# Kernel optimization log

Hardware: AMD Instinct MI355X
Metric: run time of the kernel (lower is better)

The kernel has to match this reference:

```python
import math
import jax, jax.numpy as jnp
import numpy as np

N_EMBD = 768
N_HEAD = 12
BLOCK_SIZE = 1024
B, T, N_ENC = 8, 1024, 257
EPS = 1e-5


def _ln(x, g, b):
    m = jnp.mean(x, axis=-1, keepdims=True)
    v = jnp.var(x, axis=-1, keepdims=True)
    return (x - m) * jax.lax.rsqrt(v + EPS) * g + b


def _heads(t, n_head):
    B_, N_, C_ = t.shape
    return t.reshape(B_, N_, n_head, C_ // n_head).transpose(0, 2, 1, 3)  # [B,H,N,D]


def setup_inputs() -> dict:
    key = jax.random.key(0)
    ks = jax.random.split(key, 16)
    s = 0.02
    d, h4, dq = N_EMBD, 4 * N_EMBD, N_EMBD // 4
    inp = {
        'x': jax.random.normal(ks[0], (B, T, d), jnp.float32),
        'x_enc': jax.random.normal(ks[1], (B, N_ENC, d), jnp.float32),
        'ln1_g': jnp.ones((d,), jnp.float32), 'ln1_b': jnp.zeros((d,), jnp.float32),
        'ln2_g': jnp.ones((d,), jnp.float32), 'ln2_b': jnp.zeros((d,), jnp.float32),
        'ln3_g': jnp.ones((d,), jnp.float32), 'ln3_b': jnp.zeros((d,), jnp.float32),
        'attn_w': jax.random.normal(ks[2], (d, 3 * d), jnp.float32) * s,
        'attn_bias': jnp.zeros((3 * d,), jnp.float32),
        'attn_proj_w': jax.random.normal(ks[3], (d, d), jnp.float32) * s,
        'attn_proj_b': jnp.zeros((d,), jnp.float32),
        'img_w': jax.random.normal(ks[4], (d, 2 * d), jnp.float32) * s,
        'img_b': jnp.zeros((2 * d,), jnp.float32),
        'cap_w': jax.random.normal(ks[5], (d, d), jnp.float32) * s,
        'cap_b': jnp.zeros((d,), jnp.float32),
        'cross_proj_w': jax.random.normal(ks[6], (d, d), jnp.float32) * s,
        'cross_proj_b': jnp.zeros((d,), jnp.float32),
        'ad1_w': jax.random.normal(ks[7], (d, dq), jnp.float32) * s,
        'ad1_b': jnp.zeros((dq,), jnp.float32),
        'ad2_w': jax.random.normal(ks[8], (dq, d), jnp.float32) * s,
        'ad2_b': jnp.zeros((d,), jnp.float32),
        'fc_w': jax.random.normal(ks[9], (d, h4), jnp.float32) * s,
        'fc_b': jnp.zeros((h4,), jnp.float32),
        'mproj_w': jax.random.normal(ks[10], (h4, d), jnp.float32) * s,
        'mproj_b': jnp.zeros((d,), jnp.float32),
    }
    return inp


def _block(x, x_enc, ln1_g, ln1_b, ln2_g, ln2_b, ln3_g, ln3_b,
           attn_w, attn_bias, attn_proj_w, attn_proj_b,
           img_w, img_b, cap_w, cap_b, cross_proj_w, cross_proj_b,
           ad1_w, ad1_b, ad2_w, ad2_b, fc_w, fc_b, mproj_w, mproj_b):
    d, nh = N_EMBD, N_HEAD
    hd = d // nh
    scale = 1.0 / math.sqrt(hd)

    def adapter(h):
        return jax.nn.relu(h @ ad1_w + ad1_b) @ ad2_w + ad2_b

    # --- causal self-attention ---
    h = _ln(x, ln1_g, ln1_b)
    qkv = h @ attn_w + attn_bias
    q, k, v = jnp.split(qkv, 3, axis=2)
    q, k, v = _heads(q, nh), _heads(k, nh), _heads(v, nh)  # [B,H,T,hd]
    att = jnp.einsum('bhqd,bhkd->bhqk', q, k) * scale
    Tq = x.shape[1]
    causal = jnp.tril(jnp.ones((Tq, Tq), bool))
    att = jnp.where(causal, att, -jnp.inf)
    att = jax.nn.softmax(att, axis=-1)
    sa = jnp.einsum('bhqk,bhkd->bhqd', att, v).transpose(0, 2, 1, 3).reshape(x.shape)
    sa = sa @ attn_proj_w + attn_proj_b
    x = x + adapter(sa)

    # --- cross-attention (queries from x, keys/values from x_enc) ---
    hq = _ln(x, ln1_g, ln1_b)
    he = _ln(x_enc, ln3_g, ln3_b)
    kv = he @ img_w + img_b
    k2, v2 = jnp.split(kv, 2, axis=2)
    q2 = hq @ cap_w + cap_b
    q2, k2, v2 = _heads(q2, nh), _heads(k2, nh), _heads(v2, nh)
    catt = jax.nn.softmax(jnp.einsum('bhqd,bhkd->bhqk', q2, k2) * scale, axis=-1)
    ca = jnp.einsum('bhqk,bhkd->bhqd', catt, v2).transpose(0, 2, 1, 3).reshape(x.shape)
    ca = ca @ cross_proj_w + cross_proj_b
    x = x + adapter(ca)

    # --- MLP ---
    hm = _ln(x, ln2_g, ln2_b)
    m = jax.nn.gelu(hm @ fc_w + fc_b, approximate=True) @ mproj_w + mproj_b
    x = x + adapter(m)
    return x, x_enc


def reference(x, x_enc, ln1_g, ln1_b, ln2_g, ln2_b, ln3_g, ln3_b,
              attn_w, attn_bias, attn_proj_w, attn_proj_b,
              img_w, img_b, cap_w, cap_b, cross_proj_w, cross_proj_b,
              ad1_w, ad1_b, ad2_w, ad2_b, fc_w, fc_b, mproj_w, mproj_b):
    return _block(x, x_enc, ln1_g, ln1_b, ln2_g, ln2_b, ln3_g, ln3_b,
                  attn_w, attn_bias, attn_proj_w, attn_proj_b,
                  img_w, img_b, cap_w, cap_b, cross_proj_w, cross_proj_b,
                  ad1_w, ad1_b, ad2_w, ad2_b, fc_w, fc_b, mproj_w, mproj_b)
```

## Files before the change

### kernel.cpp

```cpp
#include <hip/hip_runtime.h>

typedef unsigned short u16;
typedef short bf16x8 __attribute__((ext_vector_type(8)));
typedef float f32x4 __attribute__((ext_vector_type(4)));
typedef unsigned short u16x4 __attribute__((ext_vector_type(4)));

__device__ __forceinline__ u16 f2bf(float f) {
  union { float f; unsigned u; } v; v.f = f;
  unsigned u = v.u;
  unsigned r = (u + 0x7FFFu + ((u >> 16) & 1u)) >> 16;
  return (u16)r;
}
__device__ __forceinline__ float bf2f(u16 h) {
  union { unsigned u; float f; } v; v.u = ((unsigned)h) << 16;
  return v.f;
}
__device__ __forceinline__ float gelu_f(float x) {
  float u = (x * x * 0.044715f + 1.0f) * x * -1.5957691216057308f;
  return x / (1.0f + __expf(u));
}

#define GLD_LDS16(gp, lp)                                             \
  __builtin_amdgcn_global_load_lds(                                   \
      (const __attribute__((address_space(1))) void*)(gp),            \
      (__attribute__((address_space(3))) void*)(lp), 16, 0, 0)

template<int OFF>
__device__ __forceinline__ u16x4 tr16(unsigned a) {
  u16x4 d;
  asm volatile("ds_read_b64_tr_b16 %0, %1 offset:%2" : "=&v"(d) : "v"(a), "n"(OFF));
  return d;
}
__device__ __forceinline__ bf16x8 pack8(u16x4 a, u16x4 b) {
  union { u16x4 p[2]; bf16x8 v; } u;
  u.p[0] = a; u.p[1] = b;
  return u.v;
}

struct TrBatch {
  const float* W[9];
  u16* Bt[9];
  int K[9], N[9], Kpad[9], Npad[9];
  int tstart[10];
};
__global__ __launch_bounds__(256)
void transpose_all(TrBatch tb) {
  __shared__ float tile[64][65];
  const int tid = blockIdx.x;
  int mi = 0;
  while (mi < 8 && tid >= tb.tstart[mi + 1]) ++mi;
  const int lt = tid - tb.tstart[mi];
  const int tx = tb.Npad[mi] >> 6;
  const int n0 = (lt % tx) * 64;
  const int k0 = (lt / tx) * 64;
  const float* W = tb.W[mi];
  u16* Bt = tb.Bt[mi];
  const int K = tb.K[mi], N = tb.N[mi], Kpad = tb.Kpad[mi];
  const int t = threadIdx.x;
  const int c = t & 63;
  const int rb = t >> 6;
#pragma unroll
  for (int i = 0; i < 16; ++i) {
    int r = i * 4 + rb;
    float v = 0.f;
    if (k0 + r < K && n0 + c < N) v = W[(size_t)(k0 + r) * N + n0 + c];
    tile[r][c] = v;
  }
  __syncthreads();
#pragma unroll
  for (int i = 0; i < 16; ++i) {
    int r = i * 4 + rb;
    Bt[(size_t)(n0 + r) * Kpad + k0 + c] = f2bf(tile[c][r]);
  }
}

__global__ __launch_bounds__(64)
void ln_kernel(const float* __restrict__ X, const float* __restrict__ G,
               const float* __restrict__ Bv, u16* __restrict__ O, int Mreal) {
  const int row = blockIdx.x;
  const int l = threadIdx.x;
  u16* op = O + (size_t)row * 768;
  if (row >= Mreal) {
    u16x4 z = {0, 0, 0, 0};
#pragma unroll
    for (int i = 0; i < 3; ++i) *(u16x4*)(op + (i * 64 + l) * 4) = z;
    return;
  }
  const float* xp = X + (size_t)row * 768;
  float v[12];
  float s = 0.f, s2 = 0.f;
#pragma unroll
  for (int i = 0; i < 3; ++i) {
    float4 t4 = *(const float4*)(xp + (i * 64 + l) * 4);
    v[i * 4 + 0] = t4.x; v[i * 4 + 1] = t4.y; v[i * 4 + 2] = t4.z; v[i * 4 + 3] = t4.w;
    s += t4.x + t4.y + t4.z + t4.w;
    s2 += t4.x * t4.x + t4.y * t4.y + t4.z * t4.z + t4.w * t4.w;
  }
#pragma unroll
  for (int off = 32; off > 0; off >>= 1) {
    s += __shfl_xor(s, off);
    s2 += __shfl_xor(s2, off);
  }
  const float mean = s * (1.0f / 768.0f);
  const float var = s2 * (1.0f / 768.0f) - mean * mean;
  const float rstd = rsqrtf(var + 1e-5f);
#pragma unroll
  for (int i = 0; i < 3; ++i) {
    int base = (i * 64 + l) * 4;
    float4 g4 = *(const float4*)(G + base);
    float4 b4 = *(const float4*)(Bv + base);
    u16x4 o4;
    o4[0] = f2bf((v[i * 4 + 0] - mean) * rstd * g4.x + b4.x);
    o4[1] = f2bf((v[i * 4 + 1] - mean) * rstd * g4.y + b4.y);
    o4[2] = f2bf((v[i * 4 + 2] - mean) * rstd * g4.z + b4.z);
    o4[3] = f2bf((v[i * 4 + 3] - mean) * rstd * g4.w + b4.w);
    *(u16x4*)(op + base) = o4;
  }
}

template<bool DOLN, bool RESID>
__global__ __launch_bounds__(64)
void resid_ln(const float* __restrict__ S, float* __restrict__ D,
              const u16* __restrict__ P,
              const float* __restrict__ G, const float* __restrict__ Bv,
              u16* __restrict__ O) {
  const int row = blockIdx.x;
  const int l = threadIdx.x;
  const float* sp = S + (size_t)row * 768;
  float* dp = D + (size_t)row * 768;
  float v[12];
  float s = 0.f, s2 = 0.f;
#pragma unroll
  for (int i = 0; i < 3; ++i) {
    const int base = (i * 64 + l) * 4;
    float4 t4 = *(const float4*)(sp + base);
    if (RESID) {
      u16x4 p4 = *(const u16x4*)(P + (size_t)row * 768 + base);
      t4.x += bf2f(p4[0]); t4.y += bf2f(p4[1]);
      t4.z += bf2f(p4[2]); t4.w += bf2f(p4[3]);
    }
    v[i * 4 + 0] = t4.x; v[i * 4 + 1] = t4.y; v[i * 4 + 2] = t4.z; v[i * 4 + 3] = t4.w;
    s += t4.x + t4.y + t4.z + t4.w;
    s2 += t4.x * t4.x + t4.y * t4.y + t4.z * t4.z + t4.w * t4.w;
    *(float4*)(dp + base) = t4;
  }
  if (DOLN) {
#pragma unroll
    for (int off = 32; off > 0; off >>= 1) {
      s += __shfl_xor(s, off);
      s2 += __shfl_xor(s2, off);
    }
    const float mean = s * (1.0f / 768.0f);
    const float var = s2 * (1.0f / 768.0f) - mean * mean;
    const float rstd = rsqrtf(var + 1e-5f);
    u16* op = O + (size_t)row * 768;
#pragma unroll
    for (int i = 0; i < 3; ++i) {
      int base = (i * 64 + l) * 4;
      float4 g4 = *(const float4*)(G + base);
      float4 b4 = *(const float4*)(Bv + base);
      u16x4 o4;
      o4[0] = f2bf((v[i * 4 + 0] - mean) * rstd * g4.x + b4.x);
      o4[1] = f2bf((v[i * 4 + 1] - mean) * rstd * g4.y + b4.y);
      o4[2] = f2bf((v[i * 4 + 2] - mean) * rstd * g4.z + b4.z);
      o4[3] = f2bf((v[i * 4 + 3] - mean) * rstd * g4.w + b4.w);
      *(u16x4*)(op + base) = o4;
    }
  }
}

template<int MODE>
__global__ void gemm_bt(const u16* __restrict__ A, const u16* __restrict__ Bt,
                        void* __restrict__ C, const float* __restrict__ bias,
                        int K, int ldc, int nbias) {
  __shared__ u16 As[2 * 128 * 32];
  __shared__ u16 Bs[2 * 128 * 32];
  const int t = threadIdx.x;
  const int lane = t & 63;
  const int wid = t >> 6;
  const int wm = (wid >> 1) * 64;
  const int wn = (wid & 1) * 64;
  const int tm = blockIdx.x * 128;
  const int tn = blockIdx.y * 128;

  f32x4 zero = {0.f, 0.f, 0.f, 0.f};
  f32x4 acc[4][4];
#pragma unroll
  for (int i = 0; i < 4; ++i)
#pragma unroll
    for (int j = 0; j < 4; ++j) acc[i][j] = zero;

  const int rowA = lane & 15;
  const int kb = (lane >> 4) << 3;
  const int kTiles = K >> 6;
  for (int kt = 0; kt < kTiles; ++kt) {
    const int kk = kt << 6;
#pragma unroll
    for (int i = 0; i < 4; ++i) {
      const int c = i * 256 + t;
      const int r = (c >> 2) & 127;
      const int cc = ((c >> 9) << 5) + ((c & 3) << 3);
      GLD_LDS16(A + (size_t)(tm + r) * K + kk + cc, As + c * 8);
      GLD_LDS16(Bt + (size_t)(tn + r) * K + kk + cc, Bs + c * 8);
    }
    __syncthreads();
#pragma unroll
    for (int ks = 0; ks < 2; ++ks) {
      bf16x8 af[4], bfr[4];
      const int base = ks * 4096;
#pragma unroll
      for (int i = 0; i < 4; ++i) {
        af[i] = *(const bf16x8*)(As + base + (wm + i * 16 + rowA) * 32 + kb);
        bfr[i] = *(const bf16x8*)(Bs + base + (wn + i * 16 + rowA) * 32 + kb);
      }
#pragma unroll
      for (int mi = 0; mi < 4; ++mi)
#pragma unroll
        for (int ni = 0; ni < 4; ++ni)
          acc[mi][ni] = __builtin_amdgcn_mfma_f32_16x16x32_bf16(af[mi], bfr[ni], acc[mi][ni], 0, 0, 0);
    }
    __syncthreads();
  }
  const int col0 = lane & 15;
  const int row0 = (lane >> 4) << 2;
#pragma unroll
  for (int mi = 0; mi < 4; ++mi) {
#pragma unroll
    for (int ni = 0; ni < 4; ++ni) {
      int col = tn + wn + ni * 16 + col0;
      float bb = (col < nbias) ? bias[col] : 0.f;
#pragma unroll
      for (int r = 0; r < 4; ++r) {
        int row = tm + wm + mi * 16 + row0 + r;
        float v = acc[mi][ni][r] + bb;
        size_t idx = (size_t)row * ldc + col;
        if (MODE == 0) ((u16*)C)[idx] = f2bf(v);
        else if (MODE == 1) ((u16*)C)[idx] = f2bf(fmaxf(v, 0.f));
        else ((u16*)C)[idx] = f2bf(gelu_f(v));
      }
    }
  }
}

struct GemmJob {
  const u16* A; const u16* Bt; u16* C; const float* bias;
  int K, ldc, nbias, mblocks;
};
__global__ __launch_bounds__(256)
void gemm_bt_dual(GemmJob j0, GemmJob j1, int split) {
  __shared__ u16 As[2 * 128 * 32];
  __shared__ u16 Bs[2 * 128 * 32];
  const int bid = blockIdx.x;
  const GemmJob& J = (bid < split) ? j0 : j1;
  const int lb = (bid < split) ? bid : bid - split;
  const int tm = (lb % J.mblocks) * 128;
  const int tn = (lb / J.mblocks) * 128;
  const u16* A = J.A;
  const u16* Bt = J.Bt;
  const int K = J.K;

  const int t = threadIdx.x;
  const int lane = t & 63;
  const int wid = t >> 6;
  const int wm = (wid >> 1) * 64;
  const int wn = (wid & 1) * 64;

  f32x4 zero = {0.f, 0.f, 0.f, 0.f};
  f32x4 acc[4][4];
#pragma unroll
  for (int i = 0; i < 4; ++i)
#pragma unroll
    for (int j = 0; j < 4; ++j) acc[i][j] = zero;

  const int rowA = lane & 15;
  const int kb = (lane >> 4) << 3;
  const int kTiles = K >> 6;
  for (int kt = 0; kt < kTiles; ++kt) {
    const int kk = kt << 6;
#pragma unroll
    for (int i = 0; i < 4; ++i) {
      const int c = i * 256 + t;
      const int r = (c >> 2) & 127;
      const int cc = ((c >> 9) << 5) + ((c & 3) << 3);
      GLD_LDS16(A + (size_t)(tm + r) * K + kk + cc, As + c * 8);
      GLD_LDS16(Bt + (size_t)(tn + r) * K + kk + cc, Bs + c * 8);
    }
    __syncthreads();
#pragma unroll
    for (int ks = 0; ks < 2; ++ks) {
      bf16x8 af[4], bfr[4];
      const int base = ks * 4096;
#pragma unroll
      for (int i = 0; i < 4; ++i) {
        af[i] = *(const bf16x8*)(As + base + (wm + i * 16 + rowA) * 32 + kb);
        bfr[i] = *(const bf16x8*)(Bs + base + (wn + i * 16 + rowA) * 32 + kb);
      }
#pragma unroll
      for (int mi = 0; mi < 4; ++mi)
#pragma unroll
        for (int ni = 0; ni < 4; ++ni)
          acc[mi][ni] = __builtin_amdgcn_mfma_f32_16x16x32_bf16(af[mi], bfr[ni], acc[mi][ni], 0, 0, 0);
    }
    __syncthreads();
  }
  const int col0 = lane & 15;
  const int row0 = (lane >> 4) << 2;
#pragma unroll
  for (int mi = 0; mi < 4; ++mi) {
#pragma unroll
    for (int ni = 0; ni < 4; ++ni) {
      int col = tn + wn + ni * 16 + col0;
      float bb = (col < J.nbias) ? J.bias[col] : 0.f;
#pragma unroll
      for (int r = 0; r < 4; ++r) {
        int row = tm + wm + mi * 16 + row0 + r;
        J.C[(size_t)row * J.ldc + col] = f2bf(acc[mi][ni][r] + bb);
      }
    }
  }
}

template<bool CAUSAL>
__global__ __launch_bounds__(256)
void attn_mfma(const u16* __restrict__ Q, const u16* __restrict__ Kp,
               const u16* __restrict__ Vp,
               u16* __restrict__ O0, u16* __restrict__ O1, float2* __restrict__ ML,
               int seqkv, int qrs, int krs,
               long long qBatch, long long kBatch,
               int qoff, int koff, int voff) {
  __shared__ __align__(16) u16 Ks[64 * 64];
  __shared__ __align__(16) u16 Vs[4096];
  __shared__ __align__(16) u16 Ps[4][1024];
  const int t = threadIdx.x;
  const int lane = t & 63;
  const int wid = t >> 6;
  const int b = blockIdx.x / 12, h = blockIdx.x % 12;
  const int yq = CAUSAL ? ((int)gridDim.y - 1 - (int)blockIdx.y) : (int)blockIdx.y;
  const int q0 = yq * 64;
  const int colid = lane & 15;
  const int rgrp = lane >> 4;
  const int z = CAUSAL ? blockIdx.z : 0;

  int kt_begin = 0, kt_end;
  if (CAUSAL) {
    const int ntr = yq + 1;
    const int half = (ntr + 1) >> 1;
    kt_begin = z ? half : 0;
    kt_end = z ? ntr : half;
  } else {
    kt_end = (seqkv + 63) >> 6;
  }
  u16* Op = (CAUSAL && z) ? O1 : O0;

  if (CAUSAL && kt_begin >= kt_end) {
    if (colid == 0) {
#pragma unroll
      for (int r = 0; r < 4; ++r) {
        int qrow = q0 + wid * 16 + rgrp * 4 + r;
        ML[((size_t)z * 8192 + b * 1024 + qrow) * 12 + h] = make_float2(-1e30f, 0.f);
      }
    }
    return;
  }

  const u16* qp = Q + (size_t)b * qBatch + qoff + (size_t)(q0 + wid * 16 + colid) * qrs + h * 64;
  bf16x8 qa[2];
#pragma unroll
  for (int s = 0; s < 2; ++s) qa[s] = *(const bf16x8*)(qp + s * 32 + (rgrp << 3));

  f32x4 oacc[4];
#pragma unroll
  for (int i = 0; i < 4; ++i) oacc[i] = (f32x4){0.f, 0.f, 0.f, 0.f};
  float m[4] = {-1e30f, -1e30f, -1e30f, -1e30f};
  float l[4] = {0.f, 0.f, 0.f, 0.f};

  const u16* kbase = Kp + (size_t)b * kBatch + koff + h * 64;
  const u16* vbase = Vp + (size_t)b * kBatch + voff + h * 64;

  const int srr = t >> 3, sdc = t & 7;
  int kwo[2], vwo[2];
#pragma unroll
  for (int i = 0; i < 2; ++i) {
    const int r = srr + 32 * i;
    kwo[i] = r * 64 + ((sdc ^ (r & 7)) << 3);
    vwo[i] = ((sdc >> 1) << 10) + (i << 9) + (((srr >> 2) & 1) << 8)
           + (((srr >> 3) & 3) << 6) + ((srr & 3) << 4) + (((2 * sdc) & 3) << 2);
  }
  const unsigned vs_base = (unsigned)(size_t)&Vs[0] + 8u * (unsigned)lane;
  const unsigned ps_base = (unsigned)(size_t)&Ps[wid][0] + 8u * (unsigned)lane;

  bf16x8 kz[2], vz[2];
  auto LOADT = [&](int kt) {
    const int k0 = kt * 64;
#pragma unroll
    for (int i = 0; i < 2; ++i) {
      const int tk = k0 + srr + 32 * i;
      const int dc = sdc << 3;
      kz[i] = (bf16x8){0, 0, 0, 0, 0, 0, 0, 0};
      vz[i] = (bf16x8){0, 0, 0, 0, 0, 0, 0, 0};
      if (tk < seqkv) {
        kz[i] = *(const bf16x8*)(kbase + (size_t)tk * krs + dc);
        vz[i] = *(const bf16x8*)(vbase + (size_t)tk * krs + dc);
      }
    }
  };
  LOADT(kt_begin);

  constexpr float SC2 = 0.18033688011112042f;

  for (int kt = kt_begin; kt < kt_end; ++kt) {
    const int k0 = kt * 64;
#pragma unroll
    for (int i = 0; i < 2; ++i) {
      *(bf16x8*)&Ks[kwo[i]] = kz[i];
      *(bf16x8*)&Vs[vwo[i]] = vz[i];
    }
    __syncthreads();
    if (kt + 1 < kt_end) LOADT(kt + 1);

    f32x4 sacc[4];
#pragma unroll
    for (int c = 0; c < 4; ++c) sacc[c] = (f32x4){0.f, 0.f, 0.f, 0.f};
#pragma unroll
    for (int c = 0; c < 4; ++c)
#pragma unroll
      for (int s = 0; s < 2; ++s) {
        bf16x8 kf = *(const bf16x8*)&Ks[(c * 16 + colid) * 64 +
                                        ((((s << 2) + rgrp) ^ (colid & 7)) << 3)];
        sacc[c] = __builtin_amdgcn_mfma_f32_16x16x32_bf16(qa[s], kf, sacc[c], 0, 0, 0);
      }

    float sv[4][4];
    const bool domask = CAUSAL ? (kt == yq) : (kt == kt_end - 1);
#pragma unroll
    for (int c = 0; c < 4; ++c)
#pragma unroll
      for (int r = 0; r < 4; ++r) {
        float s = sacc[c][r] * SC2;
        if (domask) {
          int kv = k0 + c * 16 + colid;
          int q = q0 + wid * 16 + rgrp * 4 + r;
          if ((CAUSAL && kv > q) || (!CAUSAL && kv >= seqkv)) s = -1e30f;
        }
        sv[c][r] = s;
      }

    float newm[4], corr[4];
#pragma unroll
    for (int r = 0; r < 4; ++r) {
      float v = fmaxf(fmaxf(sv[0][r], sv[1][r]), fmaxf(sv[2][r], sv[3][r]));
#pragma unroll
      for (int off = 1; off < 16; off <<= 1) v = fmaxf(v, __shfl_xor(v, off));
      newm[r] = fmaxf(m[r], v);
      corr[r] = exp2f(m[r] - newm[r]);
      m[r] = newm[r];
    }
    float psum[4] = {0.f, 0.f, 0.f, 0.f};
#pragma unroll
    for (int c = 0; c < 4; ++c)
#pragma unroll
      for (int r = 0; r < 4; ++r) {
        float p = exp2f(sv[c][r] - newm[r]);
        sv[c][r] = p;
        psum[r] += p;
      }
#pragma unroll
    for (int r = 0; r < 4; ++r) {
#pragma unroll
      for (int off = 1; off < 16; off <<= 1) psum[r] += __shfl_xor(psum[r], off);
      l[r] = l[r] * corr[r] + psum[r];
#pragma unroll
      for (int dc2 = 0; dc2 < 4; ++dc2) oacc[dc2][r] *= corr[r];
    }

#pragma unroll
    for (int c = 0; c < 4; ++c) {
      u16x4 pp;
#pragma unroll
      for (int r = 0; r < 4; ++r) pp[r] = f2bf(sv[c][r]);
      const int pa = ((c >> 1) << 9) + (((colid >> 2) & 1) << 8)
                   + (((2 * c + (colid >> 3)) & 3) << 6) + ((colid & 3) << 4) + (rgrp << 2);
      *(u16x4*)&Ps[wid][pa] = pp;
    }
    __builtin_amdgcn_sched_barrier(0);

    u16x4 p00 = tr16<0>(ps_base);
    u16x4 p01 = tr16<512>(ps_base);
    u16x4 p10 = tr16<1024>(ps_base);
    u16x4 p11 = tr16<1536>(ps_base);
    asm volatile("s_waitcnt lgkmcnt(0)" ::: "memory");
    __builtin_amdgcn_sched_barrier(0);
    bf16x8 pf0 = pack8(p00, p01);
    bf16x8 pf1 = pack8(p10, p11);

#pragma unroll
    for (int dc2 = 0; dc2 < 4; ++dc2) {
      const unsigned va = vs_base + (unsigned)(dc2 * 2048);
      u16x4 v00 = tr16<0>(va);
      u16x4 v01 = tr16<512>(va);
      u16x4 v10 = tr16<1024>(va);
      u16x4 v11 = tr16<1536>(va);
      asm volatile("s_waitcnt lgkmcnt(0)" ::: "memory");
      __builtin_amdgcn_sched_barrier(0);
      bf16x8 vf0 = pack8(v00, v01);
      bf16x8 vf1 = pack8(v10, v11);
      oacc[dc2] = __builtin_amdgcn_mfma_f32_16x16x32_bf16(pf0, vf0, oacc[dc2], 0, 0, 0);
      oacc[dc2] = __builtin_amdgcn_mfma_f32_16x16x32_bf16(pf1, vf1, oacc[dc2], 0, 0, 0);
    }
    __syncthreads();
  }

#pragma unroll
  for (int r = 0; r < 4; ++r) {
    int qrow = q0 + wid * 16 + rgrp * 4 + r;
    u16* op = Op + ((size_t)b * 1024 + qrow) * 768 + h * 64;
    if (CAUSAL) {
#pragma unroll
      for (int dc2 = 0; dc2 < 4; ++dc2)
        op[dc2 * 16 + colid] = f2bf(oacc[dc2][r]);
      if (colid == 0)
        ML[((size_t)z * 8192 + b * 1024 + qrow) * 12 + h] = make_float2(m[r], l[r]);
    } else {
      float inv = 1.f / l[r];
#pragma unroll
      for (int dc2 = 0; dc2 < 4; ++dc2)
        op[dc2 * 16 + colid] = f2bf(oacc[dc2][r] * inv);
    }
  }
}

__global__ __launch_bounds__(64)
void attn_combine(const u16* __restrict__ P0, const u16* __restrict__ P1,
                  const float2* __restrict__ ML, u16* __restrict__ O) {
  const int row = blockIdx.x;
  const int l = threadIdx.x;
#pragma unroll
  for (int i = 0; i < 3; ++i) {
    const int base = (i * 64 + l) * 4;
    const int h = base >> 6;
    float2 ml0 = ML[(size_t)row * 12 + h];
    float2 ml1 = ML[(size_t)8192 * 12 + row * 12 + h];
    float mm = fmaxf(ml0.x, ml1.x);
    float w0 = exp2f(ml0.x - mm);
    float w1 = exp2f(ml1.x - mm);
    float inv = 1.f / (ml0.y * w0 + ml1.y * w1);
    u16x4 a = *(const u16x4*)(P0 + (size_t)row * 768 + base);
    u16x4 c = *(const u16x4*)(P1 + (size_t)row * 768 + base);
    u16x4 o4;
#pragma unroll
    for (int j = 0; j < 4; ++j)
      o4[j] = f2bf((bf2f(a[j]) * w0 + bf2f(c[j]) * w1) * inv);
    *(u16x4*)(O + (size_t)row * 768 + base) = o4;
  }
}

extern "C" void kernel_launch(void* const* d_in, const int* in_sizes, int n_in,
                              void* d_out, int out_size, void* d_ws, size_t ws_size,
                              hipStream_t stream) {
  const float* x        = (const float*)d_in[0];
  const float* x_enc    = (const float*)d_in[1];
  const float* ln1_g    = (const float*)d_in[2];
  const float* ln1_b    = (const float*)d_in[3];
  const float* ln2_g    = (const float*)d_in[4];
  const float* ln2_b    = (const float*)d_in[5];
  const float* ln3_g    = (const float*)d_in[6];
  const float* ln3_b    = (const float*)d_in[7];
  const float* attn_w   = (const float*)d_in[8];
  const float* attn_bias= (const float*)d_in[9];
  const float* proj_w   = (const float*)d_in[10];
  const float* proj_b   = (const float*)d_in[11];
  const float* img_w    = (const float*)d_in[12];
  const float* img_b    = (const float*)d_in[13];
  const float* cap_w    = (const float*)d_in[14];
  const float* cap_b    = (const float*)d_in[15];
  const float* cross_w  = (const float*)d_in[16];
  const float* cross_b  = (const float*)d_in[17];
  const float* ad1_w    = (const float*)d_in[18];
  const float* ad1_b    = (const float*)d_in[19];
  const float* ad2_w    = (const float*)d_in[20];
  const float* ad2_b    = (const float*)d_in[21];
  const float* fc_w     = (const float*)d_in[22];
  const float* fc_b     = (const float*)d_in[23];
  const float* mproj_w  = (const float*)d_in[24];
  const float* mproj_b  = (const float*)d_in[25];

  const int Mx = 8192;
  const int Me = 2056;
  const int MeP = 2176;

  float* out_x  = (float*)d_out;
  float* out_xe = out_x + (size_t)Mx * 768;

  char* ws = (char*)d_ws;
  size_t off = 0;
  auto alloc = [&](size_t elems) {
    u16* p = (u16*)(ws + off);
    off = (off + elems * 2 + 255) & ~(size_t)255;
    return p;
  };
  u16* wt_attn  = alloc((size_t)2304 * 768);
  u16* wt_proj  = alloc((size_t)768 * 768);
  u16* wt_img   = alloc((size_t)1536 * 768);
  u16* wt_cap   = alloc((size_t)768 * 768);
  u16* wt_cross = alloc((size_t)768 * 768);
  u16* wt_ad1   = alloc((size_t)256 * 768);
  u16* wt_ad2   = alloc((size_t)768 * 256);
  u16* wt_fc    = alloc((size_t)3072 * 768);
  u16* wt_mproj = alloc((size_t)768 * 3072);
  u16* hbuf     = alloc((size_t)Mx * 768);
  u16* big      = alloc((size_t)Mx * 3072);
  u16* p0       = alloc((size_t)Mx * 768);
  u16* p1       = alloc((size_t)Mx * 768);
  u16* hid      = alloc((size_t)Mx * 256);
  float2* mlbuf = (float2*)alloc((size_t)2 * 8192 * 12 * 4);
  u16* q2  = big;
  u16* kvb = big + (size_t)Mx * 768;

  hipMemcpyAsync(out_xe, x_enc, (size_t)Me * 768 * 4, hipMemcpyDeviceToDevice, stream);

  TrBatch tb;
  int nt = 0;
  tb.tstart[0] = 0;
  auto addT = [&](const float* W, u16* Bt, int K, int N, int Kp, int Np) {
    tb.W[nt] = W; tb.Bt[nt] = Bt; tb.K[nt] = K; tb.N[nt] = N;
    tb.Kpad[nt] = Kp; tb.Npad[nt] = Np;
    tb.tstart[nt + 1] = tb.tstart[nt] + (Np / 64) * (Kp / 64);
    ++nt;
  };
  addT(attn_w, wt_attn, 768, 2304, 768, 2304);
  addT(proj_w, wt_proj, 768, 768, 768, 768);
  addT(img_w, wt_img, 768, 1536, 768, 1536);
  addT(cap_w, wt_cap, 768, 768, 768, 768);
  addT(cross_w, wt_cross, 768, 768, 768, 768);
  addT(ad1_w, wt_ad1, 768, 192, 768, 256);
  addT(ad2_w, wt_ad2, 192, 768, 256, 768);
  addT(fc_w, wt_fc, 768, 3072, 768, 3072);
  addT(mproj_w, wt_mproj, 3072, 768, 3072, 768);
  transpose_all<<<tb.tstart[9], 256, 0, stream>>>(tb);

  auto GEMM = [&](const u16* A, const u16* Bt, void* C, const float* bias,
                  int M, int N, int K, int ldc, int nbias, int mode) {
    dim3 g(M / 128, N / 128);
    if (mode == 0)      gemm_bt<0><<<g, 256, 0, stream>>>(A, Bt, C, bias, K, ldc, nbias);
    else if (mode == 1) gemm_bt<1><<<g, 256, 0, stream>>>(A, Bt, C, bias, K, ldc, nbias);
    else                gemm_bt<2><<<g, 256, 0, stream>>>(A, Bt, C, bias, K, ldc, nbias);
  };
  auto ADAPTER = [&](const u16* in, u16* padw) {
    GEMM(in, wt_ad1, hid, ad1_b, Mx, 256, 768, 256, 192, 1);
    GEMM(hid, wt_ad2, padw, ad2_b, Mx, 768, 256, 768, 768, 0);
  };

  resid_ln<true, false><<<Mx, 64, 0, stream>>>(x, out_x, nullptr, ln1_g, ln1_b, hbuf);

  GEMM(hbuf, wt_attn, big, attn_bias, Mx, 2304, 768, 2304, 2304, 0);
  attn_mfma<true><<<dim3(96, 16, 2), 256, 0, stream>>>(
      big, big, big, hbuf, p1, mlbuf, 1024, 2304, 2304,
      (long long)1024 * 2304, (long long)1024 * 2304, 0, 768, 1536);
  attn_combine<<<Mx, 64, 0, stream>>>(hbuf, p1, mlbuf, p0);
  GEMM(p0, wt_proj, p1, proj_b, Mx, 768, 768, 768, 768, 0);
  ADAPTER(p1, p0);
  resid_ln<true, true><<<Mx, 64, 0, stream>>>(out_x, out_x, p0, ln1_g, ln1_b, hbuf);

  ln_kernel<<<MeP, 64, 0, stream>>>(x_enc, ln3_g, ln3_b, p0, Me);
  {
    GemmJob jkv = { p0,   wt_img, kvb, img_b, 768, 1536, 1536, MeP / 128 };
    GemmJob jq2 = { hbuf, wt_cap, q2,  cap_b, 768, 768,  768,  Mx / 128 };
    const int split = (MeP / 128) * (1536 / 128);
    const int total = split + (Mx / 128) * (768 / 128);
    gemm_bt_dual<<<total, 256, 0, stream>>>(jkv, jq2, split);
  }
  attn_mfma<false><<<dim3(96, 16), 256, 0, stream>>>(
      q2, kvb, kvb, p1, nullptr, nullptr, 257, 768, 1536,
      (long long)1024 * 768, (long long)257 * 1536, 0, 0, 768);
  GEMM(p1, wt_cross, p0, cross_b, Mx, 768, 768, 768, 768, 0);
  ADAPTER(p0, p1);
  resid_ln<true, true><<<Mx, 64, 0, stream>>>(out_x, out_x, p1, ln2_g, ln2_b, hbuf);

  GEMM(hbuf, wt_fc, big, fc_b, Mx, 3072, 768, 3072, 3072, 2);
  GEMM(big, wt_mproj, p0, mproj_b, Mx, 768, 3072, 768, 768, 0);
  ADAPTER(p0, p1);
  resid_ln<false, true><<<Mx, 64, 0, stream>>>(out_x, out_x, p1, nullptr, nullptr, nullptr);

  (void)in_sizes; (void)n_in; (void)out_size; (void)ws_size;
}
```

Measured before the change: 483.7 us.

## Double-buffer LDS in GEMM kernels to overlap global loads with MFMA

Adds a double-buffered LDS pipeline to gemm_bt (as a template option) and gemm_bt_dual. The next K tile is issued via global_load_lds while the current one feeds MFMAs, with a partial vmcnt wait and raw s_barrier. The intent is to hide global memory latency behind compute. GEMM dispatch picks the prefetch variant only when the grid has at most 640 blocks, since doubled LDS (64KB) lowers occupancy for large grids. Global pointer offsets are also hoisted out of the K loop.

```diff
diff --git a/kernel.cpp b/kernel.cpp
--- a/kernel.cpp
+++ b/kernel.cpp
@@ -169,12 +169,13 @@
   }
 }
 
-template<int MODE>
-__global__ void gemm_bt(const u16* __restrict__ A, const u16* __restrict__ Bt,
-                        void* __restrict__ C, const float* __restrict__ bias,
-                        int K, int ldc, int nbias) {
-  __shared__ u16 As[2 * 128 * 32];
-  __shared__ u16 Bs[2 * 128 * 32];
+template<int MODE, int PF>
+__global__ __launch_bounds__(256)
+void gemm_bt(const u16* __restrict__ A, const u16* __restrict__ Bt,
+             void* __restrict__ C, const float* __restrict__ bias,
+             int K, int ldc, int nbias) {
+  __shared__ u16 As[PF ? 2 : 1][2 * 128 * 32];
+  __shared__ u16 Bs[PF ? 2 : 1][2 * 128 * 32];
   const int t = threadIdx.x;
   const int lane = t & 63;
   const int wid = t >> 6;
@@ -190,37 +191,83 @@
 #pragma unroll
     for (int j = 0; j < 4; ++j) acc[i][j] = zero;
 
+  const u16* agp[4]; const u16* bgp[4]; int lofs[4];
+#pragma unroll
+  for (int i = 0; i < 4; ++i) {
+    const int c = i * 256 + t;
+    const int r = (c >> 2) & 127;
+    const int cc = ((c >> 9) << 5) + ((c & 3) << 3);
+    agp[i] = A + (size_t)(tm + r) * K + cc;
+    bgp[i] = Bt + (size_t)(tn + r) * K + cc;
+    lofs[i] = c * 8;
+  }
+  auto STAGE = [&](int buf, int kt) {
+    const int kk = kt << 6;
+#pragma unroll
+    for (int i = 0; i < 4; ++i) {
+      GLD_LDS16(agp[i] + kk, &As[buf][lofs[i]]);
+      GLD_LDS16(bgp[i] + kk, &Bs[buf][lofs[i]]);
+    }
+  };
+
   const int rowA = lane & 15;
   const int kb = (lane >> 4) << 3;
   const int kTiles = K >> 6;
-  for (int kt = 0; kt < kTiles; ++kt) {
-    const int kk = kt << 6;
-#pragma unroll
-    for (int i = 0; i < 4; ++i) {
-      const int c = i * 256 + t;
-      const int r = (c >> 2) & 127;
-      const int cc = ((c >> 9) << 5) + ((c & 3) << 3);
-      GLD_LDS16(A + (size_t)(tm + r) * K + kk + cc, As + c * 8);
-      GLD_LDS16(Bt + (size_t)(tn + r) * K + kk + cc, Bs + c * 8);
-    }
-    __syncthreads();
-#pragma unroll
-    for (int ks = 0; ks < 2; ++ks) {
-      bf16x8 af[4], bfr[4];
-      const int base = ks * 4096;
-#pragma unroll
-      for (int i = 0; i < 4; ++i) {
-        af[i] = *(const bf16x8*)(As + base + (wm + i * 16 + rowA) * 32 + kb);
-        bfr[i] = *(const bf16x8*)(Bs + base + (wn + i * 16 + rowA) * 32 + kb);
-      }
-#pragma unroll
-      for (int mi = 0; mi < 4; ++mi)
-#pragma unroll
-        for (int ni = 0; ni < 4; ++ni)
-          acc[mi][ni] = __builtin_amdgcn_mfma_f32_16x16x32_bf16(af[mi], bfr[ni], acc[mi][ni], 0, 0, 0);
-    }
-    __syncthreads();
-  }
+
+  if (PF) {
+    STAGE(0, 0);
+    int cur = 0;
+    for (int kt = 0; kt < kTiles; ++kt) {
+      if (kt + 1 < kTiles) {
+        STAGE(cur ^ 1, kt + 1);
+        asm volatile("s_waitcnt vmcnt(8)" ::: "memory");
+      } else {
+        asm volatile("s_waitcnt vmcnt(0)" ::: "memory");
+      }
+      __builtin_amdgcn_s_barrier();
+      __builtin_amdgcn_sched_barrier(0);
+#pragma unroll
+      for (int ks = 0; ks < 2; ++ks) {
+        bf16x8 af[4], bfr[4];
+        const int base = ks * 4096;
+#pragma unroll
+        for (int i = 0; i < 4; ++i) {
+          af[i] = *(const bf16x8*)(&As[cur][base + (wm + i * 16 + rowA) * 32 + kb]);
+          bfr[i] = *(const bf16x8*)(&Bs[cur][base + (wn + i * 16 + rowA) * 32 + kb]);
+        }
+#pragma unroll
+        for (int mi = 0; mi < 4; ++mi)
+#pragma unroll
+          for (int ni = 0; ni < 4; ++ni)
+            acc[mi][ni] = __builtin_amdgcn_mfma_f32_16x16x32_bf16(af[mi], bfr[ni], acc[mi][ni], 0, 0, 0);
+      }
+      __builtin_amdgcn_sched_barrier(0);
+      __builtin_amdgcn_s_barrier();
+      cur ^= 1;
+    }
+  } else {
+    for (int kt = 0; kt < kTiles; ++kt) {
+      STAGE(0, kt);
+      __syncthreads();
+#pragma unroll
+      for (int ks = 0; ks < 2; ++ks) {
+        bf16x8 af[4], bfr[4];
+        const int base = ks * 4096;
+#pragma unroll
+        for (int i = 0; i < 4; ++i) {
+          af[i] = *(const bf16x8*)(&As[0][base + (wm + i * 16 + rowA) * 32 + kb]);
+          bfr[i] = *(const bf16x8*)(&Bs[0][base + (wn + i * 16 + rowA) * 32 + kb]);
+        }
+#pragma unroll
+        for (int mi = 0; mi < 4; ++mi)
+#pragma unroll
+          for (int ni = 0; ni < 4; ++ni)
+            acc[mi][ni] = __builtin_amdgcn_mfma_f32_16x16x32_bf16(af[mi], bfr[ni], acc[mi][ni], 0, 0, 0);
+      }
+      __syncthreads();
+    }
+  }
+
   const int col0 = lane & 15;
   const int row0 = (lane >> 4) << 2;
 #pragma unroll
@@ -248,8 +295,8 @@
 };
 __global__ __launch_bounds__(256)
 void gemm_bt_dual(GemmJob j0, GemmJob j1, int split) {
-  __shared__ u16 As[2 * 128 * 32];
-  __shared__ u16 Bs[2 * 128 * 32];
+  __shared__ u16 As[2][2 * 128 * 32];
+  __shared__ u16 Bs[2][2 * 128 * 32];
   const int bid = blockIdx.x;
   const GemmJob& J = (bid < split) ? j0 : j1;
   const int lb = (bid < split) ? bid : bid - split;
@@ -272,28 +319,48 @@
 #pragma unroll
     for (int j = 0; j < 4; ++j) acc[i][j] = zero;
 
+  const u16* agp[4]; const u16* bgp[4]; int lofs[4];
+#pragma unroll
+  for (int i = 0; i < 4; ++i) {
+    const int c = i * 256 + t;
+    const int r = (c >> 2) & 127;
+    const int cc = ((c >> 9) << 5) + ((c & 3) << 3);
+    agp[i] = A + (size_t)(tm + r) * K + cc;
+    bgp[i] = Bt + (size_t)(tn + r) * K + cc;
+    lofs[i] = c * 8;
+  }
+  auto STAGE = [&](int buf, int kt) {
+    const int kk = kt << 6;
+#pragma unroll
+    for (int i = 0; i < 4; ++i) {
+      GLD_LDS16(agp[i] + kk, &As[buf][lofs[i]]);
+      GLD_LDS16(bgp[i] + kk, &Bs[buf][lofs[i]]);
+    }
+  };
+
   const int rowA = lane & 15;
   const int kb = (lane >> 4) << 3;
   const int kTiles = K >> 6;
+
+  STAGE(0, 0);
+  int cur = 0;
   for (int kt = 0; kt < kTiles; ++kt) {
-    const int kk = kt << 6;
-#pragma unroll
-    for (int i = 0; i < 4; ++i) {
-      const int c = i * 256 + t;
-      const int r = (c >> 2) & 127;
-      const int cc = ((c >> 9) << 5) + ((c & 3) << 3);
-      GLD_LDS16(A + (size_t)(tm + r) * K + kk + cc, As + c * 8);
-      GLD_LDS16(Bt + (size_t)(tn + r) * K + kk + cc, Bs + c * 8);
-    }
-    __syncthreads();
+    if (kt + 1 < kTiles) {
+      STAGE(cur ^ 1, kt + 1);
+      asm volatile("s_waitcnt vmcnt(8)" ::: "memory");
+    } else {
+      asm volatile("s_waitcnt vmcnt(0)" ::: "memory");
+    }
+    __builtin_amdgcn_s_barrier();
+    __builtin_amdgcn_sched_barrier(0);
 #pragma unroll
     for (int ks = 0; ks < 2; ++ks) {
       bf16x8 af[4], bfr[4];
       const int base = ks * 4096;
 #pragma unroll
       for (int i = 0; i < 4; ++i) {
-        af[i] = *(const bf16x8*)(As + base + (wm + i * 16 + rowA) * 32 + kb);
-        bfr[i] = *(const bf16x8*)(Bs + base + (wn + i * 16 + rowA) * 32 + kb);
+        af[i] = *(const bf16x8*)(&As[cur][base + (wm + i * 16 + rowA) * 32 + kb]);
+        bfr[i] = *(const bf16x8*)(&Bs[cur][base + (wn + i * 16 + rowA) * 32 + kb]);
       }
 #pragma unroll
       for (int mi = 0; mi < 4; ++mi)
@@ -301,7 +368,9 @@
         for (int ni = 0; ni < 4; ++ni)
           acc[mi][ni] = __builtin_amdgcn_mfma_f32_16x16x32_bf16(af[mi], bfr[ni], acc[mi][ni], 0, 0, 0);
     }
-    __syncthreads();
+    __builtin_amdgcn_sched_barrier(0);
+    __builtin_amdgcn_s_barrier();
+    cur ^= 1;
   }
   const int col0 = lane & 15;
   const int row0 = (lane >> 4) << 2;
@@ -641,9 +710,17 @@
   auto GEMM = [&](const u16* A, const u16* Bt, void* C, const float* bias,
                   int M, int N, int K, int ldc, int nbias, int mode) {
     dim3 g(M / 128, N / 128);
-    if (mode == 0)      gemm_bt<0><<<g, 256, 0, stream>>>(A, Bt, C, bias, K, ldc, nbias);
-    else if (mode == 1) gemm_bt<1><<<g, 256, 0, stream>>>(A, Bt, C, bias, K, ldc, nbias);
-    else                gemm_bt<2><<<g, 256, 0, stream>>>(A, Bt, C, bias, K, ldc, nbias);
+    const bool pf = (g.x * g.y) <= 640;
+    if (mode == 0) {
+      if (pf) gemm_bt<0, 1><<<g, 256, 0, stream>>>(A, Bt, C, bias, K, ldc, nbias);
+      else    gemm_bt<0, 0><<<g, 256, 0, stream>>>(A, Bt, C, bias, K, ldc, nbias);
+    } else if (mode == 1) {
+      if (pf) gemm_bt<1, 1><<<g, 256, 0, stream>>>(A, Bt, C, bias, K, ldc, nbias);
+      else    gemm_bt<1, 0><<<g, 256, 0, stream>>>(A, Bt, C, bias, K, ldc, nbias);
+    } else {
+      if (pf) gemm_bt<2, 1><<<g, 256, 0, stream>>>(A, Bt, C, bias, K, ldc, nbias);
+      else    gemm_bt<2, 0><<<g, 256, 0, stream>>>(A, Bt, C, bias, K, ldc, nbias);
+    }
   };
   auto ADAPTER = [&](const u16* in, u16* padw) {
     GEMM(in, wt_ad1, hid, ad1_b, Mx, 256, 768, 256, 192, 1);
```

New measurement: 501.2 us. 3.6% more time.
